# Optimization experiments

Measured on AMD Instinct MI355X. Metric: run time of the kernel, lower is better.

Reference implementation:

```python
import jax, jax.numpy as jnp
import numpy as np

N, E = 50000, 800000          # nodes, edges
IN_DIM, HID, OUT = 200, 256, 64  # hidden_dims
R = 2                          # num_relations
NEG_SLOPE = 0.2                # RGATConv default negative_slope
EPS = 1e-16                    # PyG softmax denominator eps


def _glorot(key, shape, fan):
    return jax.random.normal(key, shape, dtype=jnp.float32) / np.float32(np.sqrt(fan))


def setup_inputs() -> dict:
    key = jax.random.key(0)
    ks = jax.random.split(key, 13)
    features = jax.random.normal(ks[0], (N, IN_DIM), dtype=jnp.float32)
    edge_index = jax.random.randint(ks[1], (2, E), 0, N, dtype=jnp.int64)
    edge_type = jax.random.randint(ks[2], (E,), 0, R, dtype=jnp.int64)
    return {
        "features": features,
        "edge_index": edge_index,
        "edge_type": edge_type,
        # RGATConv layer 1 (heads=1, dim=1): weight [R, in, out], q/k [out, 1]
        "w1": _glorot(ks[3], (R, IN_DIM, HID), IN_DIM),
        "q1": _glorot(ks[4], (HID, 1), HID),
        "k1": _glorot(ks[5], (HID, 1), HID),
        # RGATConv layer 2
        "w2": _glorot(ks[6], (R, HID, OUT), HID),
        "q2": _glorot(ks[7], (OUT, 1), OUT),
        "k2": _glorot(ks[8], (OUT, 1), OUT),
        # decoder: Linear(OUT->HID) then Linear(HID->IN_DIM), stored as [in, out]
        "dW1": _glorot(ks[9], (OUT, HID), OUT),
        "db1": jnp.zeros((HID,), jnp.float32),
        "dW2": _glorot(ks[10], (HID, IN_DIM), HID),
        "db2": jnp.zeros((IN_DIM,), jnp.float32),
    }


def rgat_conv(x, src, dst, etype, w, q, k):
    """PyG RGATConv: additive-self-attention, across-relation softmax,
    heads=1, dim=1, concat=False, bias=False, aggr=add (eval mode: no dropout)."""
    n = x.shape[0]
    # relation-specific transform at node level (per-edge bmm factors through nodes)
    xw = jnp.einsum('ni,ric->rnc', x, w)          # [R, N, C]
    qn = jnp.einsum('rnc,ch->rnh', xw, q)         # [R, N, 1]
    kn = jnp.einsum('rnc,ch->rnh', xw, k)         # [R, N, 1]
    # per-edge attention logit: leaky_relu(q_i + k_j)
    alpha = jax.nn.leaky_relu(qn[etype, dst] + kn[etype, src], NEG_SLOPE)  # [E, 1]
    # segment softmax over destination nodes (across relations)
    m = jax.lax.stop_gradient(jax.ops.segment_max(alpha, dst, num_segments=n))
    m = jnp.where(jnp.isfinite(m), m, jnp.float32(0.0))
    ea = jnp.exp(alpha - m[dst])
    denom = jax.ops.segment_sum(ea, dst, num_segments=n)
    att = ea / (denom[dst] + EPS)                 # [E, 1]
    # scatter-add weighted messages
    msg = att * xw[etype, src]                    # [E, C]
    return jax.ops.segment_sum(msg, dst, num_segments=n)  # [N, C]


def reference(features, edge_index, edge_type, w1, q1, k1, w2, q2, k2, dW1, db1, dW2, db2):
    src, dst = edge_index[0], edge_index[1]
    h1 = jax.nn.elu(rgat_conv(features, src, dst, edge_type, w1, q1, k1))
    h2 = jax.nn.elu(rgat_conv(h1, src, dst, edge_type, w2, q2, k2))
    h3 = (h2 @ dW1 + db1) @ dW2 + db2   # decoder (PCA mode: no ReLU)
    return (h2, h3)
```

## Files before the change

### kernel.cpp

```cpp
#include <hip/hip_runtime.h>

#define IN_DIM 200
#define HID    256
#define OUT_D  64
#define RREL   2
#define NEG_SLOPE 0.2f
#define NNODE  50000
#define MPAD   50048

typedef __attribute__((ext_vector_type(8))) short bf16x8;
typedef __attribute__((ext_vector_type(4))) float f32x4;
typedef __attribute__((ext_vector_type(4))) unsigned int u32x4;

__device__ __forceinline__ float bf2f(unsigned short u) {
    union { unsigned int i; float f; } v; v.i = ((unsigned int)u) << 16; return v.f;
}
__device__ __forceinline__ unsigned short f2bf(float f) {
    union { float f; unsigned int i; } v; v.f = f;
    unsigned int u = v.i;
    return (unsigned short)((u + 0x7FFFu + ((u >> 16) & 1u)) >> 16);
}
__device__ __forceinline__ float elu(float v) { return v > 0.f ? v : (__expf(v) - 1.0f); }

__global__ void feat_cvt(const float* __restrict__ in, unsigned short* __restrict__ out)
{
    long long idx = (long long)blockIdx.x * 256 + threadIdx.x;
    int row = (int)(idx >> 6);
    int c4  = ((int)idx & 63) << 2;
    if (row >= MPAD) return;
    unsigned short v[4];
    #pragma unroll
    for (int i = 0; i < 4; ++i) {
        int c = c4 + i;
        float f = (row < NNODE && c < IN_DIM) ? in[(long long)row * IN_DIM + c] : 0.f;
        v[i] = f2bf(f);
    }
    *(ushort4*)(out + (long long)row * 256 + c4) = make_ushort4(v[0], v[1], v[2], v[3]);
}

__global__ void wt_cvt(const float* __restrict__ in, unsigned short* __restrict__ out,
                       int Kreal, int Nreal, int Kpad, int Npad, int nb)
{
    long long total = (long long)nb * Npad * Kpad;
    long long idx = (long long)blockIdx.x * 256 + threadIdx.x;
    if (idx >= total) return;
    int kk = (int)(idx % Kpad);
    long long t = idx / Kpad;
    int nrow = (int)(t % Npad);
    int z = (int)(t / Npad);
    float f = (kk < Kreal && nrow < Nreal) ? in[((long long)z * Kreal + kk) * Nreal + nrow] : 0.f;
    out[idx] = f2bf(f);
}

template<bool OUT_BF16>
__global__ __launch_bounds__(256) void gemm_mfma(
    const unsigned short* __restrict__ A,
    const unsigned short* __restrict__ Bt,
    const float* __restrict__ bias,
    void* __restrict__ Cout,
    int M, int Nn, int Kp, int Npad,
    long long strideC)
{
    __shared__ __align__(16) char lds[49152];
    const int tid  = threadIdx.x;
    const int lane = tid & 63;
    const int w    = tid >> 6;
    const int m0   = blockIdx.x * 128;
    const int n0   = blockIdx.y * 64;
    const int z    = blockIdx.z;

    const char* Ab = (const char*)A;
    const char* Bb = (const char*)(Bt + (long long)z * Npad * Kp);
    const int rs = Kp * 2;

    f32x4 acc[2][4];
    #pragma unroll
    for (int i = 0; i < 2; ++i)
        #pragma unroll
        for (int j = 0; j < 4; ++j) acc[i][j] = (f32x4){0.f, 0.f, 0.f, 0.f};

    const int KT = Kp >> 6;

    auto stage = [&](int buf, int kt) {
        char* lA = lds + buf * 24576;
        char* lB = lA + 16384;
        #pragma unroll
        for (int i = 0; i < 4; ++i) {
            int g = i * 256 + tid;
            int row = g >> 3, c = g & 7;
            const char* src = Ab + (long long)(m0 + row) * rs + kt * 128 + ((c ^ (row & 7)) << 4);
            __builtin_amdgcn_global_load_lds((const __attribute__((address_space(1))) void*)src,
                                             (__attribute__((address_space(3))) void*)(lA + g * 16),
                                             16, 0, 0);
        }
        #pragma unroll
        for (int i = 0; i < 2; ++i) {
            int g = i * 256 + tid;
            int row = g >> 3, c = g & 7;
            const char* src = Bb + (long long)(n0 + row) * rs + kt * 128 + ((c ^ (row & 7)) << 4);
            __builtin_amdgcn_global_load_lds((const __attribute__((address_space(1))) void*)src,
                                             (__attribute__((address_space(3))) void*)(lB + g * 16),
                                             16, 0, 0);
        }
    };

    stage(0, 0);
    int cur = 0;
    for (int kt = 0; kt < KT; ++kt) {
        __syncthreads();
        if (kt + 1 < KT) stage(cur ^ 1, kt + 1);
        const char* lA = lds + cur * 24576;
        const char* lB = lA + 16384;
        #pragma unroll
        for (int ks = 0; ks < 2; ++ks) {
            const int kg = ks * 4 + (lane >> 4);
            bf16x8 a[2], b[4];
            #pragma unroll
            for (int mi = 0; mi < 2; ++mi) {
                int row = w * 32 + mi * 16 + (lane & 15);
                a[mi] = *(const bf16x8*)(lA + row * 128 + ((kg ^ (row & 7)) << 4));
            }
            #pragma unroll
            for (int nj = 0; nj < 4; ++nj) {
                int row = nj * 16 + (lane & 15);
                b[nj] = *(const bf16x8*)(lB + row * 128 + ((kg ^ (row & 7)) << 4));
            }
            #pragma unroll
            for (int mi = 0; mi < 2; ++mi)
                #pragma unroll
                for (int nj = 0; nj < 4; ++nj)
                    acc[mi][nj] = __builtin_amdgcn_mfma_f32_16x16x32_bf16(a[mi], b[nj], acc[mi][nj], 0, 0, 0);
        }
        cur ^= 1;
    }

    const int colb = n0 + (lane & 15);
    #pragma unroll
    for (int mi = 0; mi < 2; ++mi) {
        #pragma unroll
        for (int nj = 0; nj < 4; ++nj) {
            int col = colb + nj * 16;
            if (col >= Nn) continue;
            float badd = bias ? bias[col] : 0.f;
            #pragma unroll
            for (int r = 0; r < 4; ++r) {
                int rowm = m0 + w * 32 + mi * 16 + ((lane >> 4) << 2) + r;
                if (rowm >= M) continue;
                float v = acc[mi][nj][r] + badd;
                if (OUT_BF16)
                    ((unsigned short*)Cout)[strideC * z + (long long)rowm * Nn + col] = f2bf(v);
                else
                    ((float*)Cout)[strideC * z + (long long)rowm * Nn + col] = v;
            }
        }
    }
}

template<int C>
__global__ __launch_bounds__(256) void qk_bf16(
    const unsigned short* __restrict__ xw, const float* __restrict__ q,
    const float* __restrict__ k, float* __restrict__ qn, float* __restrict__ kn, int n)
{
    int wv = ((blockIdx.x << 8) + threadIdx.x) >> 6;
    int lane = threadIdx.x & 63;
    if (wv >= 2 * n) return;
    int r = wv >= n;
    int node = wv - r * n;
    const unsigned short* row = xw + ((long long)r * MPAD + node) * C;
    float sq, sk;
    if (C == 256) {
        ushort4 v = *(const ushort4*)(row + lane * 4);
        float4 qv = *(const float4*)(q + lane * 4);
        float4 kv = *(const float4*)(k + lane * 4);
        float x0 = bf2f(v.x), x1 = bf2f(v.y), x2 = bf2f(v.z), x3 = bf2f(v.w);
        sq = x0 * qv.x + x1 * qv.y + x2 * qv.z + x3 * qv.w;
        sk = x0 * kv.x + x1 * kv.y + x2 * kv.z + x3 * kv.w;
    } else {
        float x = bf2f(row[lane]);
        sq = x * q[lane];
        sk = x * k[lane];
    }
    #pragma unroll
    for (int off = 32; off; off >>= 1) {
        sq += __shfl_xor(sq, off);
        sk += __shfl_xor(sk, off);
    }
    if (lane == 0) { qn[wv] = sq; kn[wv] = sk; }
}

__global__ void count_kernel(const int* __restrict__ dst, int* __restrict__ deg, int E)
{
    int e = blockIdx.x * 256 + threadIdx.x;
    if (e < E) atomicAdd(&deg[dst[e]], 1);
}

__global__ __launch_bounds__(256) void scan_blocksum(
    const int* __restrict__ deg, int* __restrict__ bsum, int n)
{
    __shared__ int red[256];
    int i = blockIdx.x * 256 + threadIdx.x;
    int v = (i < n) ? deg[i] : 0;
    red[threadIdx.x] = v;
    __syncthreads();
    #pragma unroll
    for (int off = 128; off; off >>= 1) {
        if (threadIdx.x < off) red[threadIdx.x] += red[threadIdx.x + off];
        __syncthreads();
    }
    if (threadIdx.x == 0) bsum[blockIdx.x] = red[0];
}

__global__ __launch_bounds__(256) void scan_bsum(int* __restrict__ bsum, int nb)
{
    __shared__ int buf[256];
    const int t = threadIdx.x;
    int v = (t < nb) ? bsum[t] : 0;
    buf[t] = v;
    __syncthreads();
    #pragma unroll
    for (int off = 1; off < 256; off <<= 1) {
        int u = (t >= off) ? buf[t - off] : 0;
        __syncthreads();
        buf[t] += u;
        __syncthreads();
    }
    if (t < nb) bsum[t] = buf[t] - v;
}

__global__ __launch_bounds__(256) void scan_final(
    const int* __restrict__ deg, const int* __restrict__ bsum,
    int* __restrict__ row_ptr, int* __restrict__ cursor, int n)
{
    __shared__ int buf[256];
    const int t = threadIdx.x;
    const int i = blockIdx.x * 256 + t;
    int v = (i < n) ? deg[i] : 0;
    buf[t] = v;
    __syncthreads();
    #pragma unroll
    for (int off = 1; off < 256; off <<= 1) {
        int u = (t >= off) ? buf[t - off] : 0;
        __syncthreads();
        buf[t] += u;
        __syncthreads();
    }
    int excl = bsum[blockIdx.x] + buf[t] - v;
    if (i < n) { row_ptr[i] = excl; cursor[i] = excl; }
    if (i == n - 1) row_ptr[n] = excl + v;
}

__global__ void scatter_kernel(const int* __restrict__ dst, const int* __restrict__ src,
                               const int* __restrict__ etype, int* __restrict__ cursor,
                               int* __restrict__ epk, int E)
{
    int e = blockIdx.x * 256 + threadIdx.x;
    if (e < E) {
        int d = dst[e];
        int p = atomicAdd(&cursor[d], 1);
        epk[p] = src[e] | (etype[e] << 16);
    }
}

template<int C, bool DUAL>
__global__ __launch_bounds__(256) void aggregate(
    const unsigned short* __restrict__ xw,
    const float* __restrict__ qn,
    const float* __restrict__ kn,
    const int* __restrict__ row_ptr,
    const int* __restrict__ epk,
    unsigned short* __restrict__ outb,
    float* __restrict__ outf,
    int n)
{
    constexpr int LPE   = C / 8;
    constexpr int NSLOT = 64 / LPE;

    const int wv   = ((blockIdx.x << 8) + threadIdx.x) >> 6;
    const int lane = threadIdx.x & 63;
    if (wv >= n) return;
    const int d = wv;
    const int start = row_ptr[d];
    const int end   = row_ptr[d + 1];
    const float q0 = qn[d];
    const float q1 = qn[n + d];

    float mx = -INFINITY;
    for (int j = start + lane; j < end; j += 64) {
        int p = epk[j];
        int et = p >> 16, s = p & 0xFFFF;
        float a = (et ? q1 : q0) + kn[et * n + s];
        a = a > 0.f ? a : NEG_SLOPE * a;
        mx = fmaxf(mx, a);
    }
    #pragma unroll
    for (int off = 32; off; off >>= 1) mx = fmaxf(mx, __shfl_xor(mx, off));

    float se = 0.f, ev0 = 0.f;
    {
        int c = 0;
        for (int base = start; base < end; base += 64, ++c) {
            int j = base + lane;
            float ev = 0.f;
            if (j < end) {
                int p = epk[j];
                int et = p >> 16, s = p & 0xFFFF;
                float a = (et ? q1 : q0) + kn[et * n + s];
                a = a > 0.f ? a : NEG_SLOPE * a;
                ev = __expf(a - mx);
            }
            if (c == 0) ev0 = ev;
            se += ev;
        }
    }
    #pragma unroll
    for (int off = 32; off; off >>= 1) se += __shfl_xor(se, off);
    const float inv = 1.f / (se + 1e-16f);

    const int slot = lane / LPE;
    const int hl   = lane % LPE;
    float accA[8], accB[8];
    #pragma unroll
    for (int i = 0; i < 8; ++i) { accA[i] = 0.f; accB[i] = 0.f; }

    int c = 0;
    for (int base = start; base < end; base += 64, ++c) {
        const int cnt = min(64, end - base);
        int pv = 0; float wvv = 0.f;
        if (lane < cnt) {
            pv = epk[base + lane];
            if (c == 0) {
                wvv = ev0 * inv;
            } else {
                int et = pv >> 16, s = pv & 0xFFFF;
                float a = (et ? q1 : q0) + kn[et * n + s];
                a = a > 0.f ? a : NEG_SLOPE * a;
                wvv = __expf(a - mx) * inv;
            }
        }

        const int iters = (cnt + NSLOT - 1) / NSLOT;
        int k = 0;
        for (; k + 2 <= iters; k += 2) {
            const int e0 = slot + k * NSLOT;
            const int e1 = e0 + NSLOT;
            int   pA = __shfl(pv, e0);
            float wA = __shfl(wvv, e0);
            int   pB = __shfl(pv, e1);
            float wB = __shfl(wvv, e1);
            const u32x4 rA = *(const u32x4*)(xw + ((pA >> 16) * (MPAD * C) + (pA & 0xFFFF) * C + hl * 8));
            const u32x4 rB = *(const u32x4*)(xw + ((pB >> 16) * (MPAD * C) + (pB & 0xFFFF) * C + hl * 8));
            #pragma unroll
            for (int t2 = 0; t2 < 4; ++t2) {
                unsigned dA = rA[t2], dB = rB[t2];
                accA[2 * t2]     = fmaf(wA, __uint_as_float(dA << 16),         accA[2 * t2]);
                accA[2 * t2 + 1] = fmaf(wA, __uint_as_float(dA & 0xFFFF0000u), accA[2 * t2 + 1]);
                accB[2 * t2]     = fmaf(wB, __uint_as_float(dB << 16),         accB[2 * t2]);
                accB[2 * t2 + 1] = fmaf(wB, __uint_as_float(dB & 0xFFFF0000u), accB[2 * t2 + 1]);
            }
        }
        if (k < iters) {
            const int e0 = slot + k * NSLOT;
            int   pA = __shfl(pv, e0);
            float wA = __shfl(wvv, e0);
            const u32x4 rA = *(const u32x4*)(xw + ((pA >> 16) * (MPAD * C) + (pA & 0xFFFF) * C + hl * 8));
            #pragma unroll
            for (int t2 = 0; t2 < 4; ++t2) {
                unsigned dA = rA[t2];
                accA[2 * t2]     = fmaf(wA, __uint_as_float(dA << 16),         accA[2 * t2]);
                accA[2 * t2 + 1] = fmaf(wA, __uint_as_float(dA & 0xFFFF0000u), accA[2 * t2 + 1]);
            }
        }
    }

    float acc[8];
    #pragma unroll
    for (int i = 0; i < 8; ++i) acc[i] = accA[i] + accB[i];

    #pragma unroll
    for (int off = LPE; off < 64; off <<= 1)
        #pragma unroll
        for (int t2 = 0; t2 < 8; ++t2) acc[t2] += __shfl_xor(acc[t2], off);

    if (slot == 0) {
        float fo[8];
        #pragma unroll
        for (int t2 = 0; t2 < 8; ++t2) fo[t2] = elu(acc[t2]);
        u32x4 pack;
        #pragma unroll
        for (int t2 = 0; t2 < 4; ++t2)
            pack[t2] = (unsigned)f2bf(fo[2 * t2]) | ((unsigned)f2bf(fo[2 * t2 + 1]) << 16);
        *(u32x4*)(outb + (long long)d * C + hl * 8) = pack;
        if (DUAL) {
            *(float4*)(outf + (long long)d * C + hl * 8)     = make_float4(fo[0], fo[1], fo[2], fo[3]);
            *(float4*)(outf + (long long)d * C + hl * 8 + 4) = make_float4(fo[4], fo[5], fo[6], fo[7]);
        }
    }
}

extern "C" void kernel_launch(void* const* d_in, const int* in_sizes, int n_in,
                              void* d_out, int out_size, void* d_ws, size_t ws_size,
                              hipStream_t stream)
{
    const float* features = (const float*)d_in[0];
    const int*   ei       = (const int*)d_in[1];
    const int*   etype    = (const int*)d_in[2];
    const float* w1       = (const float*)d_in[3];
    const float* q1       = (const float*)d_in[4];
    const float* k1       = (const float*)d_in[5];
    const float* w2       = (const float*)d_in[6];
    const float* q2       = (const float*)d_in[7];
    const float* k2       = (const float*)d_in[8];
    const float* dW1      = (const float*)d_in[9];
    const float* db1      = (const float*)d_in[10];
    const float* dW2      = (const float*)d_in[11];
    const float* db2      = (const float*)d_in[12];

    const int n = in_sizes[0] / IN_DIM;
    const int E = in_sizes[2];
    const int* src = ei;
    const int* dst = ei + E;

    float* out_h2 = (float*)d_out;
    float* out_h3 = out_h2 + (long long)n * OUT_D;

    char* wp = (char*)d_ws;
    auto carve = [&](size_t bytes) {
        char* p = wp; wp += (bytes + 255) & ~(size_t)255; return p;
    };
    unsigned short* A1   = (unsigned short*)carve((size_t)MPAD * 256 * 2);
    unsigned short* xw1  = (unsigned short*)carve((size_t)2 * MPAD * 256 * 2);
    unsigned short* h1   = (unsigned short*)carve((size_t)MPAD * 256 * 2);
    unsigned short* xw2  = (unsigned short*)carve((size_t)2 * MPAD * 64 * 2);
    unsigned short* h2b  = (unsigned short*)carve((size_t)MPAD * 64 * 2);
    unsigned short* tdec = (unsigned short*)carve((size_t)MPAD * 256 * 2);
    unsigned short* w1t  = (unsigned short*)carve((size_t)2 * 256 * 256 * 2);
    unsigned short* w2t  = (unsigned short*)carve((size_t)2 * 64 * 256 * 2);
    unsigned short* dW1t = (unsigned short*)carve((size_t)256 * 64 * 2);
    unsigned short* dW2t = (unsigned short*)carve((size_t)256 * 256 * 2);
    float* qnb    = (float*)carve((size_t)2 * n * 4);
    float* knb    = (float*)carve((size_t)2 * n * 4);
    int* row_ptr  = (int*)carve((size_t)(n + 1) * 4);
    int* cursor   = (int*)carve((size_t)n * 4);
    int* deg      = (int*)carve((size_t)n * 4);
    int* bsum     = (int*)carve((size_t)256 * 4);
    int* epk      = (int*)carve((size_t)E * 4);

    const int EB = (E + 255) / 256;
    const int NB = (n + 255) / 256;
    const int MB = (n + 127) / 128;
    const int WAVE_N  = (n + 3) / 4;
    const int WAVE_RN = (2 * n + 3) / 4;

    hipMemsetAsync(deg, 0, (size_t)n * sizeof(int), stream);
    count_kernel<<<EB, 256, 0, stream>>>(dst, deg, E);
    scan_blocksum<<<NB, 256, 0, stream>>>(deg, bsum, n);
    scan_bsum<<<1, 256, 0, stream>>>(bsum, NB);
    scan_final<<<NB, 256, 0, stream>>>(deg, bsum, row_ptr, cursor, n);
    scatter_kernel<<<EB, 256, 0, stream>>>(dst, src, etype, cursor, epk, E);

    feat_cvt<<<(MPAD * 64 + 255) / 256, 256, 0, stream>>>(features, A1);
    wt_cvt<<<(2 * 256 * 256 + 255) / 256, 256, 0, stream>>>(w1, w1t, IN_DIM, HID, 256, 256, RREL);
    wt_cvt<<<(2 * 64 * 256 + 255) / 256, 256, 0, stream>>>(w2, w2t, HID, OUT_D, 256, 64, RREL);
    wt_cvt<<<(256 * 64 + 255) / 256, 256, 0, stream>>>(dW1, dW1t, OUT_D, HID, 64, 256, 1);
    wt_cvt<<<(256 * 256 + 255) / 256, 256, 0, stream>>>(dW2, dW2t, HID, IN_DIM, 256, 256, 1);

    {
        dim3 g(MB, 4, RREL);
        gemm_mfma<true><<<g, 256, 0, stream>>>(A1, w1t, nullptr, xw1,
                                               n, HID, 256, 256, (long long)MPAD * HID);
    }
    qk_bf16<HID><<<WAVE_RN, 256, 0, stream>>>(xw1, q1, k1, qnb, knb, n);
    aggregate<HID, false><<<WAVE_N, 256, 0, stream>>>(xw1, qnb, knb, row_ptr, epk,
                                                      h1, nullptr, n);

    {
        dim3 g(MB, 1, RREL);
        gemm_mfma<true><<<g, 256, 0, stream>>>(h1, w2t, nullptr, xw2,
                                               n, OUT_D, 256, 64, (long long)MPAD * OUT_D);
    }
    qk_bf16<OUT_D><<<WAVE_RN, 256, 0, stream>>>(xw2, q2, k2, qnb, knb, n);
    aggregate<OUT_D, true><<<WAVE_N, 256, 0, stream>>>(xw2, qnb, knb, row_ptr, epk,
                                                       h2b, out_h2, n);

    {
        dim3 g(MB, 4, 1);
        gemm_mfma<true><<<g, 256, 0, stream>>>(h2b, dW1t, db1, tdec,
                                               n, HID, 64, 256, 0);
    }
    {
        dim3 g(MB, 4, 1);
        gemm_mfma<false><<<g, 256, 0, stream>>>(tdec, dW2t, db2, out_h3,
                                                n, IN_DIM, 256, 256, 0);
    }
}
```

Before: 373.9 us.

## Aggregate raw features before layer-1 transform using relation-sorted CSR and stacked weights

Layer 1 is reordered: attention logits come from features dotted with precomputed W·q and W·k vectors. Raw bf16 features, not the per-relation transformed rows, are aggregated into per-relation sums, concatenated into a 512-wide buffer, and multiplied once by the stacked weight matrix with ELU fused into the GEMM epilogue. The CSR is now split by relation per destination node, so the relation bit is no longer packed into edge entries. This removes the big two-relation layer-1 GEMM and the 256-wide gather of transformed rows, in exchange for a wider K GEMM, a 512-wide intermediate buffer and a larger scan.

```diff
diff --git a/kernel.cpp b/kernel.cpp
--- a/kernel.cpp
+++ b/kernel.cpp
@@ -52,7 +52,73 @@
     out[idx] = f2bf(f);
 }
 
-template<bool OUT_BF16>
+__global__ void wt_cvt_stack(const float* __restrict__ in, unsigned short* __restrict__ out)
+{
+    int idx = blockIdx.x * 256 + threadIdx.x;
+    if (idx >= 2 * 256 * 256) return;
+    int kk = idx & 255;
+    int c  = (idx >> 8) & 255;
+    int z  = idx >> 16;
+    float f = (kk < IN_DIM) ? in[((long long)z * IN_DIM + kk) * 256 + c] : 0.f;
+    out[(long long)c * 512 + z * 256 + kk] = f2bf(f);
+}
+
+__global__ __launch_bounds__(256) void wqk_cvt(
+    const float* __restrict__ w, const float* __restrict__ q,
+    const float* __restrict__ k, float* __restrict__ wqv, float* __restrict__ wkv)
+{
+    int wv = ((blockIdx.x << 8) + threadIdx.x) >> 6;
+    int lane = threadIdx.x & 63;
+    if (wv >= 512) return;
+    int r = wv >> 8, kk = wv & 255;
+    float sq = 0.f, sk = 0.f;
+    if (kk < IN_DIM) {
+        const float* row = w + ((long long)(r * IN_DIM + kk)) * 256;
+        float4 wv4 = *(const float4*)(row + lane * 4);
+        float4 qv4 = *(const float4*)(q + lane * 4);
+        float4 kv4 = *(const float4*)(k + lane * 4);
+        sq = wv4.x * qv4.x + wv4.y * qv4.y + wv4.z * qv4.z + wv4.w * qv4.w;
+        sk = wv4.x * kv4.x + wv4.y * kv4.y + wv4.z * kv4.z + wv4.w * kv4.w;
+        #pragma unroll
+        for (int off = 32; off; off >>= 1) {
+            sq += __shfl_xor(sq, off);
+            sk += __shfl_xor(sk, off);
+        }
+    }
+    if (lane == 0) { wqv[r * 256 + kk] = sq; wkv[r * 256 + kk] = sk; }
+}
+
+__global__ __launch_bounds__(256) void qk_feat(
+    const unsigned short* __restrict__ A1, const float* __restrict__ wqv,
+    const float* __restrict__ wkv, float* __restrict__ qn, float* __restrict__ kn, int n)
+{
+    int wv = ((blockIdx.x << 8) + threadIdx.x) >> 6;
+    int lane = threadIdx.x & 63;
+    if (wv >= n) return;
+    ushort4 v = *(const ushort4*)(A1 + (long long)wv * 256 + lane * 4);
+    float x0 = bf2f(v.x), x1 = bf2f(v.y), x2 = bf2f(v.z), x3 = bf2f(v.w);
+    float4 q0v = *(const float4*)(wqv + lane * 4);
+    float4 k0v = *(const float4*)(wkv + lane * 4);
+    float4 q1v = *(const float4*)(wqv + 256 + lane * 4);
+    float4 k1v = *(const float4*)(wkv + 256 + lane * 4);
+    float sq0 = x0 * q0v.x + x1 * q0v.y + x2 * q0v.z + x3 * q0v.w;
+    float sk0 = x0 * k0v.x + x1 * k0v.y + x2 * k0v.z + x3 * k0v.w;
+    float sq1 = x0 * q1v.x + x1 * q1v.y + x2 * q1v.z + x3 * q1v.w;
+    float sk1 = x0 * k1v.x + x1 * k1v.y + x2 * k1v.z + x3 * k1v.w;
+    #pragma unroll
+    for (int off = 32; off; off >>= 1) {
+        sq0 += __shfl_xor(sq0, off);
+        sk0 += __shfl_xor(sk0, off);
+        sq1 += __shfl_xor(sq1, off);
+        sk1 += __shfl_xor(sk1, off);
+    }
+    if (lane == 0) {
+        qn[wv] = sq0; qn[n + wv] = sq1;
+        kn[wv] = sk0; kn[n + wv] = sk1;
+    }
+}
+
+template<bool OUT_BF16, bool DO_ELU>
 __global__ __launch_bounds__(256) void gemm_mfma(
     const unsigned short* __restrict__ A,
     const unsigned short* __restrict__ Bt,
@@ -147,6 +213,7 @@
                 int rowm = m0 + w * 32 + mi * 16 + ((lane >> 4) << 2) + r;
                 if (rowm >= M) continue;
                 float v = acc[mi][nj][r] + badd;
+                if (DO_ELU) v = v > 0.f ? v : (__expf(v) - 1.0f);
                 if (OUT_BF16)
                     ((unsigned short*)Cout)[strideC * z + (long long)rowm * Nn + col] = f2bf(v);
                 else
@@ -188,10 +255,11 @@
     if (lane == 0) { qn[wv] = sq; kn[wv] = sk; }
 }
 
-__global__ void count_kernel(const int* __restrict__ dst, int* __restrict__ deg, int E)
+__global__ void count_kernel(const int* __restrict__ dst, const int* __restrict__ etype,
+                             int* __restrict__ deg2, int E)
 {
     int e = blockIdx.x * 256 + threadIdx.x;
-    if (e < E) atomicAdd(&deg[dst[e]], 1);
+    if (e < E) atomicAdd(&deg2[(dst[e] << 1) | etype[e]], 1);
 }
 
 __global__ __launch_bounds__(256) void scan_blocksum(
@@ -210,15 +278,15 @@
     if (threadIdx.x == 0) bsum[blockIdx.x] = red[0];
 }
 
-__global__ __launch_bounds__(256) void scan_bsum(int* __restrict__ bsum, int nb)
-{
-    __shared__ int buf[256];
+__global__ __launch_bounds__(512) void scan_bsum(int* __restrict__ bsum, int nb)
+{
+    __shared__ int buf[512];
     const int t = threadIdx.x;
     int v = (t < nb) ? bsum[t] : 0;
     buf[t] = v;
     __syncthreads();
     #pragma unroll
-    for (int off = 1; off < 256; off <<= 1) {
+    for (int off = 1; off < 512; off <<= 1) {
         int u = (t >= off) ? buf[t - off] : 0;
         __syncthreads();
         buf[t] += u;
@@ -250,67 +318,172 @@
 }
 
 __global__ void scatter_kernel(const int* __restrict__ dst, const int* __restrict__ src,
-                               const int* __restrict__ etype, int* __restrict__ cursor,
+                               const int* __restrict__ etype, int* __restrict__ cursor2,
                                int* __restrict__ epk, int E)
 {
     int e = blockIdx.x * 256 + threadIdx.x;
     if (e < E) {
-        int d = dst[e];
-        int p = atomicAdd(&cursor[d], 1);
-        epk[p] = src[e] | (etype[e] << 16);
-    }
-}
-
-template<int C, bool DUAL>
-__global__ __launch_bounds__(256) void aggregate(
+        int p = atomicAdd(&cursor2[(dst[e] << 1) | etype[e]], 1);
+        epk[p] = src[e];
+    }
+}
+
+__global__ __launch_bounds__(256) void aggregate_z(
+    const unsigned short* __restrict__ A1,
+    const float* __restrict__ qn,
+    const float* __restrict__ kn,
+    const int* __restrict__ row_ptr2,
+    const int* __restrict__ epk,
+    unsigned short* __restrict__ z,
+    int n)
+{
+    const int wv   = ((blockIdx.x << 8) + threadIdx.x) >> 6;
+    const int lane = threadIdx.x & 63;
+    if (wv >= n) return;
+    const int d = wv;
+    const int start = row_ptr2[2 * d];
+    const int mid   = row_ptr2[2 * d + 1];
+    const int end   = row_ptr2[2 * d + 2];
+    const float q0 = qn[d];
+    const float q1 = qn[n + d];
+
+    float mx = -INFINITY;
+    for (int j = start + lane; j < end; j += 64) {
+        int s = epk[j];
+        bool r1 = j >= mid;
+        float a = (r1 ? q1 : q0) + kn[(r1 ? n : 0) + s];
+        a = a > 0.f ? a : NEG_SLOPE * a;
+        mx = fmaxf(mx, a);
+    }
+    #pragma unroll
+    for (int off = 32; off; off >>= 1) mx = fmaxf(mx, __shfl_xor(mx, off));
+
+    float se = 0.f;
+    for (int j = start + lane; j < end; j += 64) {
+        int s = epk[j];
+        bool r1 = j >= mid;
+        float a = (r1 ? q1 : q0) + kn[(r1 ? n : 0) + s];
+        a = a > 0.f ? a : NEG_SLOPE * a;
+        se += __expf(a - mx);
+    }
+    #pragma unroll
+    for (int off = 32; off; off >>= 1) se += __shfl_xor(se, off);
+    const float inv = 1.f / (se + 1e-16f);
+
+    const int slot = lane >> 5;
+    const int hl   = lane & 31;
+
+    #pragma unroll
+    for (int seg = 0; seg < 2; ++seg) {
+        const int s0 = seg ? mid : start;
+        const int s1 = seg ? end : mid;
+        const float qr = seg ? q1 : q0;
+        const int kbase = seg ? n : 0;
+
+        float accA[8], accB[8];
+        #pragma unroll
+        for (int i = 0; i < 8; ++i) { accA[i] = 0.f; accB[i] = 0.f; }
+
+        for (int base = s0; base < s1; base += 64) {
+            const int cnt = min(64, s1 - base);
+            int pv = 0; float wvv = 0.f;
+            if (lane < cnt) {
+                pv = epk[base + lane];
+                float a = qr + kn[kbase + pv];
+                a = a > 0.f ? a : NEG_SLOPE * a;
+                wvv = __expf(a - mx) * inv;
+            }
+            const int iters = (cnt + 1) >> 1;
+            int k = 0;
+            for (; k + 2 <= iters; k += 2) {
+                const int e0 = slot + k * 2;
+                const int e1 = e0 + 2;
+                int   pA = __shfl(pv, e0);
+                float wA = __shfl(wvv, e0);
+                int   pB = __shfl(pv, e1);
+                float wB = __shfl(wvv, e1);
+                const u32x4 rA = *(const u32x4*)(A1 + (long long)pA * 256 + hl * 8);
+                const u32x4 rB = *(const u32x4*)(A1 + (long long)pB * 256 + hl * 8);
+                #pragma unroll
+                for (int t2 = 0; t2 < 4; ++t2) {
+                    unsigned dA = rA[t2], dB = rB[t2];
+                    accA[2 * t2]     = fmaf(wA, __uint_as_float(dA << 16),         accA[2 * t2]);
+                    accA[2 * t2 + 1] = fmaf(wA, __uint_as_float(dA & 0xFFFF0000u), accA[2 * t2 + 1]);
+                    accB[2 * t2]     = fmaf(wB, __uint_as_float(dB << 16),         accB[2 * t2]);
+                    accB[2 * t2 + 1] = fmaf(wB, __uint_as_float(dB & 0xFFFF0000u), accB[2 * t2 + 1]);
+                }
+            }
+            if (k < iters) {
+                const int e0 = slot + k * 2;
+                int   pA = __shfl(pv, e0);
+                float wA = __shfl(wvv, e0);
+                const u32x4 rA = *(const u32x4*)(A1 + (long long)pA * 256 + hl * 8);
+                #pragma unroll
+                for (int t2 = 0; t2 < 4; ++t2) {
+                    unsigned dA = rA[t2];
+                    accA[2 * t2]     = fmaf(wA, __uint_as_float(dA << 16),         accA[2 * t2]);
+                    accA[2 * t2 + 1] = fmaf(wA, __uint_as_float(dA & 0xFFFF0000u), accA[2 * t2 + 1]);
+                }
+            }
+        }
+
+        float acc[8];
+        #pragma unroll
+        for (int i = 0; i < 8; ++i) acc[i] = accA[i] + accB[i];
+        #pragma unroll
+        for (int t2 = 0; t2 < 8; ++t2) acc[t2] += __shfl_xor(acc[t2], 32);
+
+        if (slot == 0) {
+            u32x4 pack;
+            #pragma unroll
+            for (int t2 = 0; t2 < 4; ++t2)
+                pack[t2] = (unsigned)f2bf(acc[2 * t2]) | ((unsigned)f2bf(acc[2 * t2 + 1]) << 16);
+            *(u32x4*)(z + (long long)d * 512 + seg * 256 + hl * 8) = pack;
+        }
+    }
+}
+
+__global__ __launch_bounds__(256) void aggregate2(
     const unsigned short* __restrict__ xw,
     const float* __restrict__ qn,
     const float* __restrict__ kn,
-    const int* __restrict__ row_ptr,
+    const int* __restrict__ row_ptr2,
     const int* __restrict__ epk,
     unsigned short* __restrict__ outb,
     float* __restrict__ outf,
     int n)
 {
-    constexpr int LPE   = C / 8;
-    constexpr int NSLOT = 64 / LPE;
+    constexpr int LPE   = 8;
+    constexpr int NSLOT = 8;
 
     const int wv   = ((blockIdx.x << 8) + threadIdx.x) >> 6;
     const int lane = threadIdx.x & 63;
     if (wv >= n) return;
     const int d = wv;
-    const int start = row_ptr[d];
-    const int end   = row_ptr[d + 1];
+    const int start = row_ptr2[2 * d];
+    const int mid   = row_ptr2[2 * d + 1];
+    const int end   = row_ptr2[2 * d + 2];
     const float q0 = qn[d];
     const float q1 = qn[n + d];
 
     float mx = -INFINITY;
     for (int j = start + lane; j < end; j += 64) {
-        int p = epk[j];
-        int et = p >> 16, s = p & 0xFFFF;
-        float a = (et ? q1 : q0) + kn[et * n + s];
+        int s = epk[j];
+        bool r1 = j >= mid;
+        float a = (r1 ? q1 : q0) + kn[(r1 ? n : 0) + s];
         a = a > 0.f ? a : NEG_SLOPE * a;
         mx = fmaxf(mx, a);
     }
     #pragma unroll
     for (int off = 32; off; off >>= 1) mx = fmaxf(mx, __shfl_xor(mx, off));
 
-    float se = 0.f, ev0 = 0.f;
-    {
-        int c = 0;
-        for (int base = start; base < end; base += 64, ++c) {
-            int j = base + lane;
-            float ev = 0.f;
-            if (j < end) {
-                int p = epk[j];
-                int et = p >> 16, s = p & 0xFFFF;
-                float a = (et ? q1 : q0) + kn[et * n + s];
-                a = a > 0.f ? a : NEG_SLOPE * a;
-                ev = __expf(a - mx);
-            }
-            if (c == 0) ev0 = ev;
-            se += ev;
-        }
+    float se = 0.f;
+    for (int j = start + lane; j < end; j += 64) {
+        int s = epk[j];
+        bool r1 = j >= mid;
+        float a = (r1 ? q1 : q0) + kn[(r1 ? n : 0) + s];
+        a = a > 0.f ? a : NEG_SLOPE * a;
+        se += __expf(a - mx);
     }
     #pragma unroll
     for (int off = 32; off; off >>= 1) se += __shfl_xor(se, off);
@@ -322,20 +495,16 @@
     #pragma unroll
     for (int i = 0; i < 8; ++i) { accA[i] = 0.f; accB[i] = 0.f; }
 
-    int c = 0;
-    for (int base = start; base < end; base += 64, ++c) {
+    for (int base = start; base < end; base += 64) {
         const int cnt = min(64, end - base);
         int pv = 0; float wvv = 0.f;
         if (lane < cnt) {
-            pv = epk[base + lane];
-            if (c == 0) {
-                wvv = ev0 * inv;
-            } else {
-                int et = pv >> 16, s = pv & 0xFFFF;
-                float a = (et ? q1 : q0) + kn[et * n + s];
-                a = a > 0.f ? a : NEG_SLOPE * a;
-                wvv = __expf(a - mx) * inv;
-            }
+            int j = base + lane;
+            pv = epk[j];
+            bool r1 = j >= mid;
+            float a = (r1 ? q1 : q0) + kn[(r1 ? n : 0) + pv];
+            a = a > 0.f ? a : NEG_SLOPE * a;
+            wvv = __expf(a - mx) * inv;
         }
 
         const int iters = (cnt + NSLOT - 1) / NSLOT;
@@ -347,8 +516,10 @@
             float wA = __shfl(wvv, e0);
             int   pB = __shfl(pv, e1);
             float wB = __shfl(wvv, e1);
-            const u32x4 rA = *(const u32x4*)(xw + ((pA >> 16) * (MPAD * C) + (pA & 0xFFFF) * C + hl * 8));
-            const u32x4 rB = *(const u32x4*)(xw + ((pB >> 16) * (MPAD * C) + (pB & 0xFFFF) * C + hl * 8));
+            const long long oA = ((base + e0 >= mid) ? (long long)MPAD * 64 : 0) + (long long)pA * 64 + hl * 8;
+            const long long oB = ((base + e1 >= mid) ? (long long)MPAD * 64 : 0) + (long long)pB * 64 + hl * 8;
+            const u32x4 rA = *(const u32x4*)(xw + oA);
+            const u32x4 rB = *(const u32x4*)(xw + oB);
             #pragma unroll
             for (int t2 = 0; t2 < 4; ++t2) {
                 unsigned dA = rA[t2], dB = rB[t2];
@@ -362,7 +533,8 @@
             const int e0 = slot + k * NSLOT;
             int   pA = __shfl(pv, e0);
             float wA = __shfl(wvv, e0);
-            const u32x4 rA = *(const u32x4*)(xw + ((pA >> 16) * (MPAD * C) + (pA & 0xFFFF) * C + hl * 8));
+            const long long oA = ((base + e0 >= mid) ? (long long)MPAD * 64 : 0) + (long long)pA * 64 + hl * 8;
+            const u32x4 rA = *(const u32x4*)(xw + oA);
             #pragma unroll
             for (int t2 = 0; t2 < 4; ++t2) {
                 unsigned dA = rA[t2];
@@ -375,7 +547,6 @@
     float acc[8];
     #pragma unroll
     for (int i = 0; i < 8; ++i) acc[i] = accA[i] + accB[i];
-
     #pragma unroll
     for (int off = LPE; off < 64; off <<= 1)
         #pragma unroll
@@ -389,11 +560,9 @@
         #pragma unroll
         for (int t2 = 0; t2 < 4; ++t2)
             pack[t2] = (unsigned)f2bf(fo[2 * t2]) | ((unsigned)f2bf(fo[2 * t2 + 1]) << 16);
-        *(u32x4*)(outb + (long long)d * C + hl * 8) = pack;
-        if (DUAL) {
-            *(float4*)(outf + (long long)d * C + hl * 8)     = make_float4(fo[0], fo[1], fo[2], fo[3]);
-            *(float4*)(outf + (long long)d * C + hl * 8 + 4) = make_float4(fo[4], fo[5], fo[6], fo[7]);
-        }
+        *(u32x4*)(outb + (long long)d * 64 + hl * 8) = pack;
+        *(float4*)(outf + (long long)d * 64 + hl * 8)     = make_float4(fo[0], fo[1], fo[2], fo[3]);
+        *(float4*)(outf + (long long)d * 64 + hl * 8 + 4) = make_float4(fo[4], fo[5], fo[6], fo[7]);
     }
 }
 
@@ -417,6 +586,7 @@
 
     const int n = in_sizes[0] / IN_DIM;
     const int E = in_sizes[2];
+    const int n2 = 2 * n;
     const int* src = ei;
     const int* dst = ei + E;
 
@@ -428,68 +598,70 @@
         char* p = wp; wp += (bytes + 255) & ~(size_t)255; return p;
     };
     unsigned short* A1   = (unsigned short*)carve((size_t)MPAD * 256 * 2);
-    unsigned short* xw1  = (unsigned short*)carve((size_t)2 * MPAD * 256 * 2);
+    unsigned short* zbuf = (unsigned short*)carve((size_t)MPAD * 512 * 2);
     unsigned short* h1   = (unsigned short*)carve((size_t)MPAD * 256 * 2);
     unsigned short* xw2  = (unsigned short*)carve((size_t)2 * MPAD * 64 * 2);
     unsigned short* h2b  = (unsigned short*)carve((size_t)MPAD * 64 * 2);
     unsigned short* tdec = (unsigned short*)carve((size_t)MPAD * 256 * 2);
-    unsigned short* w1t  = (unsigned short*)carve((size_t)2 * 256 * 256 * 2);
+    unsigned short* wst  = (unsigned short*)carve((size_t)256 * 512 * 2);
     unsigned short* w2t  = (unsigned short*)carve((size_t)2 * 64 * 256 * 2);
     unsigned short* dW1t = (unsigned short*)carve((size_t)256 * 64 * 2);
     unsigned short* dW2t = (unsigned short*)carve((size_t)256 * 256 * 2);
-    float* qnb    = (float*)carve((size_t)2 * n * 4);
-    float* knb    = (float*)carve((size_t)2 * n * 4);
-    int* row_ptr  = (int*)carve((size_t)(n + 1) * 4);
-    int* cursor   = (int*)carve((size_t)n * 4);
-    int* deg      = (int*)carve((size_t)n * 4);
-    int* bsum     = (int*)carve((size_t)256 * 4);
+    float* wqv    = (float*)carve((size_t)2 * 256 * 4);
+    float* wkv    = (float*)carve((size_t)2 * 256 * 4);
+    float* qnb    = (float*)carve((size_t)n2 * 4);
+    float* knb    = (float*)carve((size_t)n2 * 4);
+    int* row_ptr2 = (int*)carve((size_t)(n2 + 1) * 4);
+    int* cursor2  = (int*)carve((size_t)n2 * 4);
+    int* deg2     = (int*)carve((size_t)n2 * 4);
+    int* bsum     = (int*)carve((size_t)512 * 4);
     int* epk      = (int*)carve((size_t)E * 4);
 
-    const int EB = (E + 255) / 256;
-    const int NB = (n + 255) / 256;
-    const int MB = (n + 127) / 128;
+    const int EB  = (E + 255) / 256;
+    const int NB2 = (n2 + 255) / 256;
+    const int MB  = (n + 127) / 128;
     const int WAVE_N  = (n + 3) / 4;
-    const int WAVE_RN = (2 * n + 3) / 4;
-
-    hipMemsetAsync(deg, 0, (size_t)n * sizeof(int), stream);
-    count_kernel<<<EB, 256, 0, stream>>>(dst, deg, E);
-    scan_blocksum<<<NB, 256, 0, stream>>>(deg, bsum, n);
-    scan_bsum<<<1, 256, 0, stream>>>(bsum, NB);
-    scan_final<<<NB, 256, 0, stream>>>(deg, bsum, row_ptr, cursor, n);
-    scatter_kernel<<<EB, 256, 0, stream>>>(dst, src, etype, cursor, epk, E);
+    const int WAVE_RN = (n2 + 3) / 4;
+
+    hipMemsetAsync(deg2, 0, (size_t)n2 * sizeof(int), stream);
+    count_kernel<<<EB, 256, 0, stream>>>(dst, etype, deg2, E);
+    scan_blocksum<<<NB2, 256, 0, stream>>>(deg2, bsum, n2);
+    scan_bsum<<<1, 512, 0, stream>>>(bsum, NB2);
+    scan_final<<<NB2, 256, 0, stream>>>(deg2, bsum, row_ptr2, cursor2, n2);
+    scatter_kernel<<<EB, 256, 0, stream>>>(dst, src, etype, cursor2, epk, E);
 
     feat_cvt<<<(MPAD * 64 + 255) / 256, 256, 0, stream>>>(features, A1);
-    wt_cvt<<<(2 * 256 * 256 + 255) / 256, 256, 0, stream>>>(w1, w1t, IN_DIM, HID, 256, 256, RREL);
+    wt_cvt_stack<<<(2 * 256 * 256 + 255) / 256, 256, 0, stream>>>(w1, wst);
     wt_cvt<<<(2 * 64 * 256 + 255) / 256, 256, 0, stream>>>(w2, w2t, HID, OUT_D, 256, 64, RREL);
     wt_cvt<<<(256 * 64 + 255) / 256, 256, 0, stream>>>(dW1, dW1t, OUT_D, HID, 64, 256, 1);
     wt_cvt<<<(256 * 256 + 255) / 256, 256, 0, stream>>>(dW2, dW2t, HID, IN_DIM, 256, 256, 1);
-
+    wqk_cvt<<<128, 256, 0, stream>>>(w1, q1, k1, wqv, wkv);
+
+    qk_feat<<<WAVE_N, 256, 0, stream>>>(A1, wqv, wkv, qnb, knb, n);
+    aggregate_z<<<WAVE_N, 256, 0, stream>>>(A1, qnb, knb, row_ptr2, epk, zbuf, n);
     {
-        dim3 g(MB, 4, RREL);
-        gemm_mfma<true><<<g, 256, 0, stream>>>(A1, w1t, nullptr, xw1,
-                                               n, HID, 256, 256, (long long)MPAD * HID);
-    }
-    qk_bf16<HID><<<WAVE_RN, 256, 0, stream>>>(xw1, q1, k1, qnb, knb, n);
-    aggregate<HID, false><<<WAVE_N, 256, 0, stream>>>(xw1, qnb, knb, row_ptr, epk,
-                                                      h1, nullptr, n);
+        dim3 g(MB, 4, 1);
+        gemm_mfma<true, true><<<g, 256, 0, stream>>>(zbuf, wst, nullptr, h1,
+                                                     n, HID, 512, 256, 0);
+    }
 
     {
         dim3 g(MB, 1, RREL);
-        gemm_mfma<true><<<g, 256, 0, stream>>>(h1, w2t, nullptr, xw2,
-                                               n, OUT_D, 256, 64, (long long)MPAD * OUT_D);
+        gemm_mfma<true, false><<<g, 256, 0, stream>>>(h1, w2t, nullptr, xw2,
+                                                      n, OUT_D, 256, 64, (long long)MPAD * OUT_D);
     }
     qk_bf16<OUT_D><<<WAVE_RN, 256, 0, stream>>>(xw2, q2, k2, qnb, knb, n);
-    aggregate<OUT_D, true><<<WAVE_N, 256, 0, stream>>>(xw2, qnb, knb, row_ptr, epk,
-                                                       h2b, out_h2, n);
+    aggregate2<<<WAVE_N, 256, 0, stream>>>(xw2, qnb, knb, row_ptr2, epk,
+                                           h2b, out_h2, n);
 
     {
         dim3 g(MB, 4, 1);
-        gemm_mfma<true><<<g, 256, 0, stream>>>(h2b, dW1t, db1, tdec,
-                                               n, HID, 64, 256, 0);
+        gemm_mfma<true, false><<<g, 256, 0, stream>>>(h2b, dW1t, db1, tdec,
+                                                      n, HID, 64, 256, 0);
     }
     {
         dim3 g(MB, 4, 1);
-        gemm_mfma<false><<<g, 256, 0, stream>>>(tdec, dW2t, db2, out_h3,
-                                                n, IN_DIM, 256, 256, 0);
-    }
-}
+        gemm_mfma<false, false><<<g, 256, 0, stream>>>(tdec, dW2t, db2, out_h3,
+                                                       n, IN_DIM, 256, 256, 0);
+    }
+}
```

Result: faster. 365.5 us (-2.2%).
